# Kernel tuning notes

Hardware: AMD Instinct MI355X
Metric: run time of the kernel (lower is better)

## Reference

```python
import jax, jax.numpy as jnp
import numpy as np
import math
from jax import lax

L, E, H, F = 4, 1024, 16, 4096
B, S = 8, 512
VV, VR = 40, 30
DIST_V = 200
PAD_ID = 0


def setup_inputs() -> dict:
    key = jax.random.key(0)
    ks = iter(jax.random.split(key, 32))
    w = lambda *sh: jax.random.normal(next(ks), sh, jnp.float32) * 0.02
    inp = {
        'val_emb': w(VV, E),
        'ring_emb': w(VR, E),
        'dist_emb': w(DIST_V, H),
        'Wqkv': w(L, 3 * E, E), 'bqkv': jnp.zeros((L, 3 * E), jnp.float32),
        'Wo': w(L, E, E), 'bo': jnp.zeros((L, E), jnp.float32),
        'ln1_s': jnp.ones((L, E), jnp.float32), 'ln1_b': jnp.zeros((L, E), jnp.float32),
        'W1': w(L, F, E), 'b1': jnp.zeros((L, F), jnp.float32),
        'W2': w(L, E, F), 'b2': jnp.zeros((L, E), jnp.float32),
        'ln2_s': jnp.ones((L, E), jnp.float32), 'ln2_b': jnp.zeros((L, E), jnp.float32),
        'lnf_s': jnp.ones((E,), jnp.float32), 'lnf_b': jnp.zeros((E,), jnp.float32),
        'gen_W': w(VV * VR, E), 'gen_b': jnp.zeros((VV * VR,), jnp.float32),
    }
    val = jax.random.randint(next(ks), (B, S), 0, VV)
    val = val.at[:, 0].set(1)  # ensure first key is never <pad> (id 0)
    inp['val_sequences'] = val
    inp['ring_sequences'] = jax.random.randint(next(ks), (B, S), 0, VR)
    inp['distance_squares'] = jax.random.randint(next(ks), (B, S, S), 0, DIST_V)
    return inp


def _ln(x, s, b):
    m = x.mean(-1, keepdims=True)
    v = ((x - m) ** 2).mean(-1, keepdims=True)
    return (x - m) / jnp.sqrt(v + 1e-5) * s + b


def _forward(val_emb, ring_emb, dist_emb, Wqkv, bqkv, Wo, bo, ln1_s, ln1_b,
             W1, b1, W2, b2, ln2_s, ln2_b, lnf_s, lnf_b, gen_W, gen_b,
             val_sequences, ring_sequences, distance_squares):
    Bv, Sv = val_sequences.shape
    dh = E // H
    scale = 1.0 / math.sqrt(dh)
    # token embeddings, each scaled by sqrt(emb_size)
    x = (val_emb[val_sequences] + ring_emb[ring_sequences]) * math.sqrt(E)  # [B,S,E]
    # distance bias [B,S,S,H] -> [B,H,S,S], causal fill with -inf, key padding -inf
    bias = jnp.transpose(dist_emb[distance_squares], (0, 3, 1, 2))
    causal = jnp.tril(jnp.ones((Sv, Sv), bool))
    mask = jnp.where(causal[None, None], bias, -jnp.inf)
    pad = (val_sequences == PAD_ID)  # [B,S]
    mask = jnp.where(pad[:, None, None, :], -jnp.inf, mask)

    def step(h, p):
        wqkv, bq, wo, bo_, l1s, l1b, w1, b1_, w2, b2_, l2s, l2b = p
        qkv = h @ wqkv.T + bq  # [B,S,3E]
        q, k, v = jnp.split(qkv, 3, axis=-1)
        q = q.reshape(Bv, Sv, H, dh).transpose(0, 2, 1, 3)
        k = k.reshape(Bv, Sv, H, dh).transpose(0, 2, 1, 3)
        v = v.reshape(Bv, Sv, H, dh).transpose(0, 2, 1, 3)
        scores = jnp.einsum('bhqd,bhkd->bhqk', q, k) * scale + mask
        a = jax.nn.softmax(scores, axis=-1)
        ctx = jnp.einsum('bhqk,bhkd->bhqd', a, v)
        ctx = ctx.transpose(0, 2, 1, 3).reshape(Bv, Sv, E)
        h = _ln(h + ctx @ wo.T + bo_, l1s, l1b)  # post-norm
        ff = jax.nn.gelu(h @ w1.T + b1_, approximate=False) @ w2.T + b2_
        h = _ln(h + ff, l2s, l2b)
        return h, None

    layer_params = (Wqkv, bqkv, Wo, bo, ln1_s, ln1_b, W1, b1, W2, b2, ln2_s, ln2_b)
    x, _ = lax.scan(step, x, layer_params)
    x = _ln(x, lnf_s, lnf_b)
    return x @ gen_W.T + gen_b  # [B,S,VV*VR]


def reference(val_emb, ring_emb, dist_emb, Wqkv, bqkv, Wo, bo, ln1_s, ln1_b,
              W1, b1, W2, b2, ln2_s, ln2_b, lnf_s, lnf_b, gen_W, gen_b,
              val_sequences, ring_sequences, distance_squares):
    return _forward(val_emb, ring_emb, dist_emb, Wqkv, bqkv, Wo, bo, ln1_s, ln1_b,
                    W1, b1, W2, b2, ln2_s, ln2_b, lnf_s, lnf_b, gen_W, gen_b,
                    val_sequences, ring_sequences, distance_squares)
```

## Files before the change

kernel.cpp:

```cpp
#include <hip/hip_runtime.h>
#include <hip/hip_bf16.h>

typedef __attribute__((ext_vector_type(8))) short bf16x8;
typedef __attribute__((ext_vector_type(4))) float f32x4;
typedef unsigned short u16;
typedef __attribute__((ext_vector_type(4))) unsigned short u16x4;

#define L_ 4
#define E_ 1024
#define H_ 16
#define F_ 4096
#define B_ 8
#define S_ 512
#define T_ 4096
#define GEN_N 1200
#define GEN_PAD 1280

#define AS1 __attribute__((address_space(1)))
#define AS3 __attribute__((address_space(3)))

static __device__ __forceinline__ u16 f2bf(float f) {
  unsigned u = __float_as_uint(f);
  unsigned r = (u + 0x7fffu + ((u >> 16) & 1u)) >> 16;
  return (u16)r;
}

static __device__ __forceinline__ float fast_gelu(float v) {
  float y = 0.7978845608f * (v + 0.044715f * v * v * v);
  y = fminf(fmaxf(y, -9.f), 9.f);
  float e2 = __expf(2.f * y);
  float th = (e2 - 1.f) / (e2 + 1.f);
  return 0.5f * v * (1.f + th);
}

__global__ __launch_bounds__(256) void cvt_bf16(const float* __restrict__ src,
                                                u16* __restrict__ dst, int n) {
  int i = (blockIdx.x * 256 + threadIdx.x) * 4;
  if (i >= n) return;
  float4 v = *reinterpret_cast<const float4*>(src + i);
  u16x4 o = {f2bf(v.x), f2bf(v.y), f2bf(v.z), f2bf(v.w)};
  *reinterpret_cast<u16x4*>(dst + i) = o;
}

__global__ __launch_bounds__(256) void embed_k(const float* __restrict__ val_emb,
                                               const float* __restrict__ ring_emb,
                                               const int* __restrict__ vseq,
                                               const int* __restrict__ rseq,
                                               float* __restrict__ h, u16* __restrict__ xbf) {
  int tok = blockIdx.x;
  int e = threadIdx.x * 4;
  int v = vseq[tok], r = rseq[tok];
  float4 a = *reinterpret_cast<const float4*>(val_emb + v * E_ + e);
  float4 b = *reinterpret_cast<const float4*>(ring_emb + r * E_ + e);
  float4 o;
  o.x = (a.x + b.x) * 32.f; o.y = (a.y + b.y) * 32.f;
  o.z = (a.z + b.z) * 32.f; o.w = (a.w + b.w) * 32.f;
  *reinterpret_cast<float4*>(h + (size_t)tok * E_ + e) = o;
  u16x4 ob = {f2bf(o.x), f2bf(o.y), f2bf(o.z), f2bf(o.w)};
  *reinterpret_cast<u16x4*>(xbf + (size_t)tok * E_ + e) = ob;
}

__global__ __launch_bounds__(256) void ln_k(const float* hin, const float* add0,
                                            const float* add1, const float* cbias,
                                            const float* g, const float* bta,
                                            float* hout, u16* xout) {
  int tok = blockIdx.x;
  int e = threadIdx.x * 4;
  float4 v = *reinterpret_cast<const float4*>(hin + (size_t)tok * E_ + e);
  if (add0) {
    float4 a0 = *reinterpret_cast<const float4*>(add0 + (size_t)tok * E_ + e);
    float4 a1 = *reinterpret_cast<const float4*>(add1 + (size_t)tok * E_ + e);
    float4 cb = *reinterpret_cast<const float4*>(cbias + e);
    v.x += a0.x + a1.x + cb.x; v.y += a0.y + a1.y + cb.y;
    v.z += a0.z + a1.z + cb.z; v.w += a0.w + a1.w + cb.w;
  }
  float s = v.x + v.y + v.z + v.w;
  float q = v.x * v.x + v.y * v.y + v.z * v.z + v.w * v.w;
  #pragma unroll
  for (int off = 1; off < 64; off <<= 1) {
    s += __shfl_xor(s, off, 64);
    q += __shfl_xor(q, off, 64);
  }
  __shared__ float ls[4], lq[4];
  int wv = threadIdx.x >> 6, ln = threadIdx.x & 63;
  if (ln == 0) { ls[wv] = s; lq[wv] = q; }
  __syncthreads();
  s = ls[0] + ls[1] + ls[2] + ls[3];
  q = lq[0] + lq[1] + lq[2] + lq[3];
  float mean = s * (1.f / E_);
  float var = q * (1.f / E_) - mean * mean;
  float inv = rsqrtf(var + 1e-5f);
  float4 gg = *reinterpret_cast<const float4*>(g + e);
  float4 bb = *reinterpret_cast<const float4*>(bta + e);
  float4 o;
  o.x = (v.x - mean) * inv * gg.x + bb.x;
  o.y = (v.y - mean) * inv * gg.y + bb.y;
  o.z = (v.z - mean) * inv * gg.z + bb.z;
  o.w = (v.w - mean) * inv * gg.w + bb.w;
  if (hout) *reinterpret_cast<float4*>(hout + (size_t)tok * E_ + e) = o;
  u16x4 ob = {f2bf(o.x), f2bf(o.y), f2bf(o.z), f2bf(o.w)};
  *reinterpret_cast<u16x4*>(xout + (size_t)tok * E_ + e) = ob;
}

template <int EPI, int NW, int SPLITK>
__global__ __launch_bounds__(512, 2) void gemm_big(const u16* __restrict__ A,
                                                   const u16* __restrict__ W,
                                                   const float* __restrict__ bias,
                                                   void* __restrict__ Cp,
                                                   u16* __restrict__ Vt,
                                                   int M, int N, int K, int tilesN) {
  constexpr int BN = 64 * NW;
  __shared__ __align__(16) u16 As[2][256 * 64];
  __shared__ __align__(16) u16 Bs[2][BN * 64];
  int tid = threadIdx.x;
  int wid = tid >> 6, ln = tid & 63;
  int wm = wid >> 2, wn = wid & 3;
  int lr = ln & 15, lk = ln >> 4;
  int nwg = gridDim.x;
  int bid = blockIdx.x;
  int swz = ((nwg & 7) == 0) ? ((bid & 7) * (nwg >> 3) + (bid >> 3)) : bid;
  int sp = 0, tile = swz;
  if (SPLITK > 1) { sp = swz & (SPLITK - 1); tile = swz / SPLITK; }
  int tm = tile / tilesN, tn = tile % tilesN;
  int row0 = tm * 256, col0 = tn * BN;
  int Ks = K / SPLITK;
  int kbase = sp * Ks;

  int srow = tid >> 3;
  int schunk = ((tid & 7) ^ (srow & 7)) * 8;
  const u16* gA = A + (size_t)(row0 + srow) * K + kbase + schunk;
  const u16* gB = W + (size_t)(col0 + srow) * K + kbase + schunk;
  size_t ldsBase = (size_t)((wid << 3) * 64) * 2;

  auto stage = [&](int buf, int kt) {
    size_t ko = (size_t)kt * 64;
    #pragma unroll
    for (int i = 0; i < 4; ++i)
      __builtin_amdgcn_global_load_lds(
          (const AS1 void*)(gA + (size_t)i * 64 * K + ko),
          (AS3 void*)((char*)&As[buf][0] + ldsBase + (size_t)i * 64 * 128), 16, 0, 0);
    #pragma unroll
    for (int i = 0; i < NW; ++i)
      __builtin_amdgcn_global_load_lds(
          (const AS1 void*)(gB + (size_t)i * 64 * K + ko),
          (AS3 void*)((char*)&Bs[buf][0] + ldsBase + (size_t)i * 64 * 128), 16, 0, 0);
  };

  f32x4 acc[8][NW];
  f32x4 z = {0.f, 0.f, 0.f, 0.f};
  #pragma unroll
  for (int m = 0; m < 8; ++m)
    #pragma unroll
    for (int n = 0; n < NW; ++n) acc[m][n] = z;

  auto compute = [&](int buf) {
    #pragma unroll
    for (int s = 0; s < 2; ++s) {
      int ch = ((s * 4 + lk) ^ (lr & 7)) * 8;
      bf16x8 bfr[NW];
      #pragma unroll
      for (int n = 0; n < NW; ++n)
        bfr[n] = *reinterpret_cast<const bf16x8*>(&Bs[buf][(wn * (16 * NW) + n * 16 + lr) * 64 + ch]);
      #pragma unroll
      for (int m = 0; m < 8; ++m) {
        bf16x8 af = *reinterpret_cast<const bf16x8*>(&As[buf][(wm * 128 + m * 16 + lr) * 64 + ch]);
        #pragma unroll
        for (int n = 0; n < NW; ++n)
          acc[m][n] = __builtin_amdgcn_mfma_f32_16x16x32_bf16(af, bfr[n], acc[m][n], 0, 0, 0);
      }
    }
  };

  int nt = Ks >> 6;
  stage(0, 0);
  int cur = 0;
  for (int t = 0; t < nt; ++t) {
    if (t + 1 < nt) {
      stage(cur ^ 1, t + 1);
      if constexpr (NW == 2) asm volatile("s_waitcnt vmcnt(6)" ::: "memory");
      else if constexpr (NW == 3) asm volatile("s_waitcnt vmcnt(7)" ::: "memory");
      else asm volatile("s_waitcnt vmcnt(8)" ::: "memory");
    } else {
      asm volatile("s_waitcnt vmcnt(0)" ::: "memory");
    }
    __builtin_amdgcn_s_barrier();
    asm volatile("" ::: "memory");
    compute(cur);
    asm volatile("" ::: "memory");
    __builtin_amdgcn_s_barrier();
    cur ^= 1;
  }

  #pragma unroll
  for (int n = 0; n < NW; ++n) {
    int col = col0 + wn * (16 * NW) + n * 16 + lr;
    if (col >= N) continue;
    float bv = (EPI == 2) ? 0.f : bias[col];
    #pragma unroll
    for (int m = 0; m < 8; ++m) {
      int rbase = row0 + wm * 128 + m * 16 + lk * 4;
      #pragma unroll
      for (int r2 = 0; r2 < 4; ++r2) {
        float v = acc[m][n][r2] + bv;
        if (EPI == 1) v = fast_gelu(v);
        int row = rbase + r2;
        if (EPI == 2)
          ((float*)Cp)[(size_t)sp * M * N + (size_t)row * N + col] = v;
        else if (EPI == 3)
          ((float*)Cp)[(size_t)row * N + col] = v;
        else {
          u16 bw = f2bf(v);
          ((u16*)Cp)[(size_t)row * N + col] = bw;
          if (EPI == 0 && Vt != nullptr && col >= 2 * E_) {
            int dg = col - 2 * E_;
            int hh = dg >> 6, dd = dg & 63;
            int bb = row >> 9, ss = row & 511;
            Vt[((size_t)((bb * 16 + hh) * 64 + dd) << 9) + ss] = bw;
          }
        }
      }
    }
  }
}

__global__ __launch_bounds__(256, 4) void attn_scores_k(const u16* __restrict__ qkv,
                                                        const int* __restrict__ dist,
                                                        const float* __restrict__ dist_emb,
                                                        const int* __restrict__ vseq,
                                                        u16* __restrict__ P,
                                                        float* __restrict__ invl) {
  int blk = blockIdx.x;
  int bh = blk & 127;
  int qt = blk >> 7;
  int b = bh >> 4, h = bh & 15;
  int tid = threadIdx.x, wv = tid >> 6, ln = tid & 63;
  int lr = ln & 15, lk = ln >> 4;

  __shared__ float de[208];
  __shared__ unsigned char padf[512];
  __shared__ unsigned char d8[64 * 512];

  int ncol = (qt + 1) * 64;
  for (int i = tid; i < 208; i += 256)
    de[i] = (i < 200) ? dist_emb[i * H_ + h] : -1e30f;
  for (int i = tid; i < (ncol >> 2); i += 256) {
    int4 v = *reinterpret_cast<const int4*>(vseq + b * S_ + i * 4);
    uchar4 pz;
    pz.x = (v.x == 0); pz.y = (v.y == 0); pz.z = (v.z == 0); pz.w = (v.w == 0);
    *reinterpret_cast<uchar4*>(&padf[i * 4]) = pz;
  }
  __syncthreads();

  {
    int r = tid >> 2;
    const int* drow = dist + ((size_t)(b * S_ + qt * 64 + r) << 9);
    int nc4 = ncol >> 2;
    for (int c4 = (tid & 3); c4 < nc4; c4 += 4) {
      int4 dv = *reinterpret_cast<const int4*>(drow + c4 * 4);
      uchar4 o;
      o.x = padf[c4 * 4 + 0] ? (unsigned char)200 : (unsigned char)dv.x;
      o.y = padf[c4 * 4 + 1] ? (unsigned char)200 : (unsigned char)dv.y;
      o.z = padf[c4 * 4 + 2] ? (unsigned char)200 : (unsigned char)dv.z;
      o.w = padf[c4 * 4 + 3] ? (unsigned char)200 : (unsigned char)dv.w;
      *reinterpret_cast<uchar4*>(&d8[(r << 9) + c4 * 4]) = o;
    }
  }
  __syncthreads();

  int q0 = qt * 64 + wv * 16;
  int nv = 4 * qt + wv + 1;
  int nreq = 4 * qt + 2 * (wv >> 1) + 2;
  int qrow = q0 + lk * 4;
  int lrow = wv * 16 + lk * 4;

  bf16x8 aq0 = *reinterpret_cast<const bf16x8*>(
      qkv + (size_t)(b * S_ + q0 + lr) * 3072 + h * 64 + lk * 8);
  bf16x8 aq1 = *reinterpret_cast<const bf16x8*>(
      qkv + (size_t)(b * S_ + q0 + lr) * 3072 + h * 64 + 32 + lk * 8);

  float sm[4] = {0.f, 0.f, 0.f, 0.f};
  f32x4 z = {0.f, 0.f, 0.f, 0.f};
  int nch = (nv + 3) >> 2;
  #pragma unroll 1
  for (int c = 0; c < nch; ++c) {
    int base = c * 4;
    f32x4 acc[4] = {z, z, z, z};
    #pragma unroll
    for (int j = 0; j < 4; ++j) {
      int n = base + j;
      if (n < nv) {
        const u16* kb = qkv + (size_t)(b * S_ + n * 16 + lr) * 3072 + E_ + h * 64 + lk * 8;
        bf16x8 bk0 = *reinterpret_cast<const bf16x8*>(kb);
        bf16x8 bk1 = *reinterpret_cast<const bf16x8*>(kb + 32);
        acc[j] = __builtin_amdgcn_mfma_f32_16x16x32_bf16(aq0, bk0, acc[j], 0, 0, 0);
        acc[j] = __builtin_amdgcn_mfma_f32_16x16x32_bf16(aq1, bk1, acc[j], 0, 0, 0);
      }
    }
    #pragma unroll
    for (int j = 0; j < 4; ++j) {
      int n = base + j;
      if (n < nv) {
        int col = n * 16 + lr;
        #pragma unroll
        for (int r2 = 0; r2 < 4; ++r2) {
          float e = 0.f;
          if (col <= qrow + r2) {
            int d = d8[((lrow + r2) << 9) + col];
            e = __expf(acc[j][r2] * 0.125f + de[d]);
          }
          sm[r2] += e;
          P[(size_t)(bh * S_ + qrow + r2) * S_ + col] = f2bf(e);
        }
      }
    }
  }
  for (int n = nv; n < nreq; ++n) {
    int col = n * 16 + lr;
    #pragma unroll
    for (int r2 = 0; r2 < 4; ++r2)
      P[(size_t)(bh * S_ + qrow + r2) * S_ + col] = 0;
  }
  #pragma unroll
  for (int off = 1; off < 16; off <<= 1)
    #pragma unroll
    for (int r2 = 0; r2 < 4; ++r2) sm[r2] += __shfl_xor(sm[r2], off, 64);
  if (lr == 0) {
    #pragma unroll
    for (int r2 = 0; r2 < 4; ++r2)
      invl[bh * S_ + qrow + r2] = 1.f / sm[r2];
  }
}

__global__ __launch_bounds__(256) void attn_pv_k(const u16* __restrict__ P,
                                                 const u16* __restrict__ Vt,
                                                 const float* __restrict__ invl,
                                                 u16* __restrict__ ctx) {
  int blk = blockIdx.x;
  int mt = blk & 3, bh = blk >> 2;
  int b = bh >> 4, h = bh & 15;
  int tid = threadIdx.x, wv = tid >> 6, ln = tid & 63;
  int lr = ln & 15, lk = ln >> 4;
  int r0 = mt * 128 + wv * 32;
  f32x4 acc[2][4];
  f32x4 z = {0.f, 0.f, 0.f, 0.f};
  #pragma unroll
  for (int m = 0; m < 2; ++m)
    #pragma unroll
    for (int n = 0; n < 4; ++n) acc[m][n] = z;
  int nks = mt * 4 + wv + 1;
  for (int ks = 0; ks < nks; ++ks) {
    int k0 = ks * 32;
    bf16x8 ap[2];
    #pragma unroll
    for (int m = 0; m < 2; ++m)
      ap[m] = *reinterpret_cast<const bf16x8*>(
          P + (size_t)(bh * S_ + r0 + m * 16 + lr) * S_ + k0 + lk * 8);
    #pragma unroll
    for (int n = 0; n < 4; ++n) {
      bf16x8 bv = *reinterpret_cast<const bf16x8*>(
          Vt + (size_t)(bh * 64 + n * 16 + lr) * S_ + k0 + lk * 8);
      #pragma unroll
      for (int m = 0; m < 2; ++m)
        acc[m][n] = __builtin_amdgcn_mfma_f32_16x16x32_bf16(ap[m], bv, acc[m][n], 0, 0, 0);
    }
  }
  float il[2][4];
  #pragma unroll
  for (int m = 0; m < 2; ++m)
    #pragma unroll
    for (int r = 0; r < 4; ++r)
      il[m][r] = invl[bh * S_ + r0 + m * 16 + lk * 4 + r];
  #pragma unroll
  for (int m = 0; m < 2; ++m)
    #pragma unroll
    for (int n = 0; n < 4; ++n)
      #pragma unroll
      for (int r = 0; r < 4; ++r) {
        int row = r0 + m * 16 + lk * 4 + r;
        int col = n * 16 + lr;
        ctx[(size_t)(b * S_ + row) * E_ + h * 64 + col] = f2bf(acc[m][n][r] * il[m][r]);
      }
}

extern "C" void kernel_launch(void* const* d_in, const int* in_sizes, int n_in,
                              void* d_out, int out_size, void* d_ws, size_t ws_size,
                              hipStream_t stream) {
  const float* val_emb = (const float*)d_in[0];
  const float* ring_emb = (const float*)d_in[1];
  const float* dist_emb = (const float*)d_in[2];
  const float* Wqkv = (const float*)d_in[3];
  const float* bqkv = (const float*)d_in[4];
  const float* Wo = (const float*)d_in[5];
  const float* bo = (const float*)d_in[6];
  const float* ln1_s = (const float*)d_in[7];
  const float* ln1_b = (const float*)d_in[8];
  const float* W1 = (const float*)d_in[9];
  const float* b1 = (const float*)d_in[10];
  const float* W2 = (const float*)d_in[11];
  const float* b2 = (const float*)d_in[12];
  const float* ln2_s = (const float*)d_in[13];
  const float* ln2_b = (const float*)d_in[14];
  const float* lnf_s = (const float*)d_in[15];
  const float* lnf_b = (const float*)d_in[16];
  const float* gen_W = (const float*)d_in[17];
  const float* gen_b = (const float*)d_in[18];
  const int* vseq = (const int*)d_in[19];
  const int* rseq = (const int*)d_in[20];
  const int* dist = (const int*)d_in[21];

  char* ws = (char*)d_ws;
  size_t off = 0;
  auto alloc = [&](size_t nbytes) {
    char* p = ws + off;
    off += (nbytes + 255) & ~(size_t)255;
    return p;
  };
  u16* gw_bf = (u16*)alloc((size_t)GEN_PAD * E_ * 2);
  u16* wqkv_l = (u16*)alloc((size_t)3 * E_ * E_ * 2);
  u16* wo_l = (u16*)alloc((size_t)E_ * E_ * 2);
  u16* w1_l = (u16*)alloc((size_t)F_ * E_ * 2);
  u16* w2_l = (u16*)alloc((size_t)E_ * F_ * 2);
  float* h = (float*)alloc((size_t)T_ * E_ * 4);
  u16* x_bf = (u16*)alloc((size_t)T_ * E_ * 2);
  u16* qkv_bf = (u16*)alloc((size_t)T_ * 3 * E_ * 2);
  u16* ctx_bf = (u16*)alloc((size_t)T_ * E_ * 2);
  u16* vt_bf = (u16*)alloc((size_t)B_ * H_ * 64 * S_ * 2);
  float* invl = (float*)alloc((size_t)B_ * H_ * S_ * 4);
  u16* p_bf = (u16*)alloc((size_t)B_ * H_ * S_ * S_ * 2);
  u16* ff_bf = p_bf;
  float* psum = (float*)(p_bf + (size_t)T_ * F_);
  (void)ws_size; (void)in_sizes; (void)n_in; (void)out_size; (void)rseq;

  auto cvt = [&](const float* s, u16* d, int n) {
    cvt_bf16<<<dim3((n / 4 + 255) / 256), dim3(256), 0, stream>>>(s, d, n);
  };
  cvt(gen_W, gw_bf, GEN_N * E_);

  embed_k<<<dim3(T_), dim3(256), 0, stream>>>(val_emb, ring_emb, vseq, rseq, h, x_bf);

  for (int l = 0; l < L_; ++l) {
    cvt(Wqkv + (size_t)l * 3 * E_ * E_, wqkv_l, 3 * E_ * E_);
    cvt(Wo + (size_t)l * E_ * E_, wo_l, E_ * E_);
    cvt(W1 + (size_t)l * F_ * E_, w1_l, F_ * E_);
    cvt(W2 + (size_t)l * E_ * F_, w2_l, E_ * F_);

    gemm_big<0, 3, 1><<<dim3(256), dim3(512), 0, stream>>>(
        x_bf, wqkv_l, bqkv + (size_t)l * 3 * E_, qkv_bf, vt_bf, T_, 3 * E_, E_, 16);
    attn_scores_k<<<dim3(B_ * H_ * 8), dim3(256), 0, stream>>>(qkv_bf, dist, dist_emb, vseq,
                                                               p_bf, invl);
    attn_pv_k<<<dim3(B_ * H_ * 4), dim3(256), 0, stream>>>(p_bf, vt_bf, invl, ctx_bf);
    gemm_big<2, 2, 2><<<dim3(256), dim3(512), 0, stream>>>(
        ctx_bf, wo_l, nullptr, psum, nullptr, T_, E_, E_, 8);
    ln_k<<<dim3(T_), dim3(256), 0, stream>>>(h, psum, psum + (size_t)T_ * E_,
                                             bo + (size_t)l * E_,
                                             ln1_s + (size_t)l * E_, ln1_b + (size_t)l * E_,
                                             h, x_bf);
    gemm_big<1, 4, 1><<<dim3(256), dim3(512), 0, stream>>>(
        x_bf, w1_l, b1 + (size_t)l * F_, ff_bf, nullptr, T_, F_, E_, 16);
    gemm_big<2, 2, 2><<<dim3(256), dim3(512), 0, stream>>>(
        ff_bf, w2_l, nullptr, psum, nullptr, T_, E_, F_, 8);
    ln_k<<<dim3(T_), dim3(256), 0, stream>>>(h, psum, psum + (size_t)T_ * E_,
                                             b2 + (size_t)l * E_,
                                             ln2_s + (size_t)l * E_, ln2_b + (size_t)l * E_,
                                             h, x_bf);
  }
  ln_k<<<dim3(T_), dim3(256), 0, stream>>>(h, nullptr, nullptr, nullptr, lnf_s, lnf_b,
                                           nullptr, x_bf);
  gemm_big<3, 2, 1><<<dim3(160), dim3(512), 0, stream>>>(
      x_bf, gw_bf, gen_b, (float*)d_out, nullptr, T_, GEN_N, E_, 10);
}
```

Measured before the change: 1.161 ms.

## Add 256x256-tile GEMM with split-K-stage pipelining for QKV and FFN layers

Adds a new gemm8 kernel that uses 256x256 output tiles, an XOR-swizzled LDS layout, and direct global-to-LDS loads. Each 64-wide K step is split into two 32-wide halves so the next half's load overlaps the current compute, and MFMA issue priority is raised during compute. The QKV, FFN1 and FFN2 GEMMs switch to it. FFN2 now uses 4-way split-K, with two extra partial buffers placed in the qkv buffer and summed in a widened LayerNorm kernel. Tradeoffs are fewer workgroups for QKV (192), higher register pressure from the larger accumulator, and extra partial-sum memory traffic for FFN2.

New measurement: 1.180 ms. Within noise of the previous version (+1.6%).

```diff
diff --git a/kernel.cpp b/kernel.cpp
--- a/kernel.cpp
+++ b/kernel.cpp
@@ -61,7 +61,8 @@
 }
 
 __global__ __launch_bounds__(256) void ln_k(const float* hin, const float* add0,
-                                            const float* add1, const float* cbias,
+                                            const float* add1, const float* add2,
+                                            const float* add3, const float* cbias,
                                             const float* g, const float* bta,
                                             float* hout, u16* xout) {
   int tok = blockIdx.x;
@@ -73,6 +74,12 @@
     float4 cb = *reinterpret_cast<const float4*>(cbias + e);
     v.x += a0.x + a1.x + cb.x; v.y += a0.y + a1.y + cb.y;
     v.z += a0.z + a1.z + cb.z; v.w += a0.w + a1.w + cb.w;
+    if (add2) {
+      float4 a2 = *reinterpret_cast<const float4*>(add2 + (size_t)tok * E_ + e);
+      float4 a3 = *reinterpret_cast<const float4*>(add3 + (size_t)tok * E_ + e);
+      v.x += a2.x + a3.x; v.y += a2.y + a3.y;
+      v.z += a2.z + a3.z; v.w += a2.w + a3.w;
+    }
   }
   float s = v.x + v.y + v.z + v.w;
   float q = v.x * v.x + v.y * v.y + v.z * v.z + v.w * v.w;
@@ -100,6 +107,145 @@
   if (hout) *reinterpret_cast<float4*>(hout + (size_t)tok * E_ + e) = o;
   u16x4 ob = {f2bf(o.x), f2bf(o.y), f2bf(o.z), f2bf(o.w)};
   *reinterpret_cast<u16x4*>(xout + (size_t)tok * E_ + e) = ob;
+}
+
+template <int EPI, int SPLITK>
+__global__ __launch_bounds__(512, 2) void gemm8(const u16* __restrict__ A,
+                                                const u16* __restrict__ W,
+                                                const float* __restrict__ bias,
+                                                void* __restrict__ Cp,
+                                                float* __restrict__ Cp2,
+                                                u16* __restrict__ Vt,
+                                                int M, int N, int K, int tilesN) {
+  __shared__ __align__(16) char lds[131072];
+  int tid = threadIdx.x;
+  int wid = tid >> 6, l = tid & 63;
+  int wm = wid >> 2, wn = wid & 3, bh = wn >> 1;
+  int lr = l & 15, lk = l >> 4;
+  int su = wid & 3;
+  int sb = (wid & 1) | ((wid >> 2) << 1);
+  int nwg = gridDim.x, bid = blockIdx.x;
+  int swz = ((nwg & 7) == 0) ? ((bid & 7) * (nwg >> 3) + (bid >> 3)) : bid;
+  int sp = 0, tile = swz;
+  if (SPLITK > 1) { sp = swz & (SPLITK - 1); tile = swz / SPLITK; }
+  int tm = tile / tilesN, tn = tile % tilesN;
+  int row0 = tm * 256, col0 = tn * 256;
+  int Ks = K / SPLITK, kbase = sp * Ks;
+
+  int arow0 = row0 + wm * 128 + su * 32 + (l >> 2);
+  int brow0 = col0 + bh * 128 + sb * 32 + (l >> 2);
+  int sch = ((l & 3) ^ ((l >> 2) & 3)) * 8;
+  const u16* gA0 = A + (size_t)arow0 * K + kbase + sch;
+  const u16* gA1 = A + (size_t)(arow0 + 16) * K + kbase + sch;
+  const u16* gB0 = W + (size_t)brow0 * K + kbase + sch;
+  const u16* gB1 = W + (size_t)(brow0 + 16) * K + kbase + sch;
+  int dA = wm * 16384 + su * 2048;
+  int dB = 65536 + bh * 16384 + sb * 2048;
+
+  auto stageU = [&](int buf, int s, int kt) {
+    size_t ko = (size_t)kt * 64 + s * 32;
+    int bo = buf * 32768 + s * 8192;
+    __builtin_amdgcn_global_load_lds((const AS1 void*)(gA0 + ko),
+                                     (AS3 void*)(lds + dA + bo), 16, 0, 0);
+    __builtin_amdgcn_global_load_lds((const AS1 void*)(gA1 + ko),
+                                     (AS3 void*)(lds + dA + bo + 1024), 16, 0, 0);
+    __builtin_amdgcn_global_load_lds((const AS1 void*)(gB0 + ko),
+                                     (AS3 void*)(lds + dB + bo), 16, 0, 0);
+    __builtin_amdgcn_global_load_lds((const AS1 void*)(gB1 + ko),
+                                     (AS3 void*)(lds + dB + bo + 1024), 16, 0, 0);
+  };
+
+  int rsw = (lk ^ (lr & 3)) * 16;
+  f32x4 acc[8][4];
+  f32x4 z = {0.f, 0.f, 0.f, 0.f};
+  #pragma unroll
+  for (int m = 0; m < 8; ++m)
+    #pragma unroll
+    for (int n = 0; n < 4; ++n) acc[m][n] = z;
+
+  int nt = Ks >> 6;
+  stageU(0, 0, 0);
+  stageU(0, 1, 0);
+  for (int t = 0; t < nt; ++t) {
+    int buf = t & 1;
+    int aoff = buf * 32768 + wm * 16384;
+    int boff = 65536 + buf * 32768 + bh * 16384 + (wn & 1) * 4096;
+    if (t + 1 < nt) {
+      stageU(buf ^ 1, 0, t + 1);
+      asm volatile("s_waitcnt vmcnt(4)" ::: "memory");
+    } else {
+      asm volatile("s_waitcnt vmcnt(0)" ::: "memory");
+    }
+    __builtin_amdgcn_s_barrier();
+    asm volatile("" ::: "memory");
+    {
+      bf16x8 bfr[4], af[8];
+      #pragma unroll
+      for (int n = 0; n < 4; ++n)
+        bfr[n] = *reinterpret_cast<const bf16x8*>(lds + boff + (n * 16 + lr) * 64 + rsw);
+      #pragma unroll
+      for (int m = 0; m < 8; ++m)
+        af[m] = *reinterpret_cast<const bf16x8*>(lds + aoff + (m * 16 + lr) * 64 + rsw);
+      __builtin_amdgcn_s_setprio(1);
+      #pragma unroll
+      for (int m = 0; m < 8; ++m)
+        #pragma unroll
+        for (int n = 0; n < 4; ++n)
+          acc[m][n] = __builtin_amdgcn_mfma_f32_16x16x32_bf16(af[m], bfr[n], acc[m][n], 0, 0, 0);
+      __builtin_amdgcn_s_setprio(0);
+    }
+    if (t + 1 < nt) stageU(buf ^ 1, 1, t + 1);
+    asm volatile("" ::: "memory");
+    __builtin_amdgcn_s_barrier();
+    asm volatile("" ::: "memory");
+    {
+      bf16x8 bfr[4], af[8];
+      #pragma unroll
+      for (int n = 0; n < 4; ++n)
+        bfr[n] = *reinterpret_cast<const bf16x8*>(lds + boff + 8192 + (n * 16 + lr) * 64 + rsw);
+      #pragma unroll
+      for (int m = 0; m < 8; ++m)
+        af[m] = *reinterpret_cast<const bf16x8*>(lds + aoff + 8192 + (m * 16 + lr) * 64 + rsw);
+      __builtin_amdgcn_s_setprio(1);
+      #pragma unroll
+      for (int m = 0; m < 8; ++m)
+        #pragma unroll
+        for (int n = 0; n < 4; ++n)
+          acc[m][n] = __builtin_amdgcn_mfma_f32_16x16x32_bf16(af[m], bfr[n], acc[m][n], 0, 0, 0);
+      __builtin_amdgcn_s_setprio(0);
+    }
+    asm volatile("" ::: "memory");
+  }
+
+  #pragma unroll
+  for (int n = 0; n < 4; ++n) {
+    int col = col0 + wn * 64 + n * 16 + lr;
+    if (col >= N) continue;
+    float bv = (EPI == 2) ? 0.f : bias[col];
+    #pragma unroll
+    for (int m = 0; m < 8; ++m) {
+      int rbase = row0 + wm * 128 + m * 16 + lk * 4;
+      #pragma unroll
+      for (int r2 = 0; r2 < 4; ++r2) {
+        float v = acc[m][n][r2] + bv;
+        if (EPI == 1) v = fast_gelu(v);
+        int row = rbase + r2;
+        if (EPI == 2) {
+          float* dst = (sp < 2) ? (float*)Cp : Cp2;
+          dst[(size_t)(sp & 1) * M * N + (size_t)row * N + col] = v;
+        } else {
+          u16 bw = f2bf(v);
+          ((u16*)Cp)[(size_t)row * N + col] = bw;
+          if (EPI == 0 && Vt != nullptr && col >= 2 * E_) {
+            int dg = col - 2 * E_;
+            int hh = dg >> 6, dd = dg & 63;
+            int bb = row >> 9, ss = row & 511;
+            Vt[((size_t)((bb * 16 + hh) * 64 + dd) << 9) + ss] = bw;
+          }
+        }
+      }
+    }
+  }
 }
 
 template <int EPI, int NW, int SPLITK>
@@ -178,7 +324,6 @@
     if (t + 1 < nt) {
       stage(cur ^ 1, t + 1);
       if constexpr (NW == 2) asm volatile("s_waitcnt vmcnt(6)" ::: "memory");
-      else if constexpr (NW == 3) asm volatile("s_waitcnt vmcnt(7)" ::: "memory");
       else asm volatile("s_waitcnt vmcnt(8)" ::: "memory");
     } else {
       asm volatile("s_waitcnt vmcnt(0)" ::: "memory");
@@ -202,25 +347,15 @@
       #pragma unroll
       for (int r2 = 0; r2 < 4; ++r2) {
         float v = acc[m][n][r2] + bv;
-        if (EPI == 1) v = fast_gelu(v);
         int row = rbase + r2;
         if (EPI == 2)
           ((float*)Cp)[(size_t)sp * M * N + (size_t)row * N + col] = v;
-        else if (EPI == 3)
+        else
           ((float*)Cp)[(size_t)row * N + col] = v;
-        else {
-          u16 bw = f2bf(v);
-          ((u16*)Cp)[(size_t)row * N + col] = bw;
-          if (EPI == 0 && Vt != nullptr && col >= 2 * E_) {
-            int dg = col - 2 * E_;
-            int hh = dg >> 6, dd = dg & 63;
-            int bb = row >> 9, ss = row & 511;
-            Vt[((size_t)((bb * 16 + hh) * 64 + dd) << 9) + ss] = bw;
-          }
-        }
       }
     }
   }
+  (void)Vt;
 }
 
 __global__ __launch_bounds__(256, 4) void attn_scores_k(const u16* __restrict__ qkv,
@@ -429,6 +564,7 @@
   u16* p_bf = (u16*)alloc((size_t)B_ * H_ * S_ * S_ * 2);
   u16* ff_bf = p_bf;
   float* psum = (float*)(p_bf + (size_t)T_ * F_);
+  float* psum2 = (float*)qkv_bf;
   (void)ws_size; (void)in_sizes; (void)n_in; (void)out_size; (void)rseq;
 
   auto cvt = [&](const float* s, u16* d, int n) {
@@ -444,28 +580,29 @@
     cvt(W1 + (size_t)l * F_ * E_, w1_l, F_ * E_);
     cvt(W2 + (size_t)l * E_ * F_, w2_l, E_ * F_);
 
-    gemm_big<0, 3, 1><<<dim3(256), dim3(512), 0, stream>>>(
-        x_bf, wqkv_l, bqkv + (size_t)l * 3 * E_, qkv_bf, vt_bf, T_, 3 * E_, E_, 16);
+    gemm8<0, 1><<<dim3(192), dim3(512), 0, stream>>>(
+        x_bf, wqkv_l, bqkv + (size_t)l * 3 * E_, qkv_bf, nullptr, vt_bf, T_, 3 * E_, E_, 12);
     attn_scores_k<<<dim3(B_ * H_ * 8), dim3(256), 0, stream>>>(qkv_bf, dist, dist_emb, vseq,
                                                                p_bf, invl);
     attn_pv_k<<<dim3(B_ * H_ * 4), dim3(256), 0, stream>>>(p_bf, vt_bf, invl, ctx_bf);
     gemm_big<2, 2, 2><<<dim3(256), dim3(512), 0, stream>>>(
         ctx_bf, wo_l, nullptr, psum, nullptr, T_, E_, E_, 8);
     ln_k<<<dim3(T_), dim3(256), 0, stream>>>(h, psum, psum + (size_t)T_ * E_,
-                                             bo + (size_t)l * E_,
+                                             nullptr, nullptr, bo + (size_t)l * E_,
                                              ln1_s + (size_t)l * E_, ln1_b + (size_t)l * E_,
                                              h, x_bf);
-    gemm_big<1, 4, 1><<<dim3(256), dim3(512), 0, stream>>>(
-        x_bf, w1_l, b1 + (size_t)l * F_, ff_bf, nullptr, T_, F_, E_, 16);
-    gemm_big<2, 2, 2><<<dim3(256), dim3(512), 0, stream>>>(
-        ff_bf, w2_l, nullptr, psum, nullptr, T_, E_, F_, 8);
+    gemm8<1, 1><<<dim3(256), dim3(512), 0, stream>>>(
+        x_bf, w1_l, b1 + (size_t)l * F_, ff_bf, nullptr, nullptr, T_, F_, E_, 16);
+    gemm8<2, 4><<<dim3(256), dim3(512), 0, stream>>>(
+        ff_bf, w2_l, nullptr, psum, psum2, nullptr, T_, E_, F_, 4);
     ln_k<<<dim3(T_), dim3(256), 0, stream>>>(h, psum, psum + (size_t)T_ * E_,
+                                             psum2, psum2 + (size_t)T_ * E_,
                                              b2 + (size_t)l * E_,
                                              ln2_s + (size_t)l * E_, ln2_b + (size_t)l * E_,
                                              h, x_bf);
   }
-  ln_k<<<dim3(T_), dim3(256), 0, stream>>>(h, nullptr, nullptr, nullptr, lnf_s, lnf_b,
-                                           nullptr, x_bf);
+  ln_k<<<dim3(T_), dim3(256), 0, stream>>>(h, nullptr, nullptr, nullptr, nullptr, nullptr,
+                                           lnf_s, lnf_b, nullptr, x_bf);
   gemm_big<3, 2, 1><<<dim3(160), dim3(512), 0, stream>>>(
       x_bf, gw_bf, gen_b, (float*)d_out, nullptr, T_, GEN_N, E_, 10);
 }
```

## Fuse attention scores and PV into one kernel keeping probabilities in registers

Applied to the files above, without the earlier changes.

Merges the score/softmax kernel and the PV kernel into a single fused attention kernel. It computes S transposed so each lane holds key-major probabilities, then packs them to bf16 and shuffles them across lanes into an MFMA A-fragment, accumulating P·V directly without writing P to global memory. This removes the large bf16 P round trip through HBM and one kernel launch per layer, and pads the LDS distance tile to avoid bank conflicts. The cost is extra cross-lane shuffles and less PV parallelism, since each block now does its query tile's full causal range serially.

Measured after the change: 1.086 ms. 6.4% less time.

```diff
diff --git a/kernel.cpp b/kernel.cpp
--- a/kernel.cpp
+++ b/kernel.cpp
@@ -23,6 +23,12 @@
   unsigned u = __float_as_uint(f);
   unsigned r = (u + 0x7fffu + ((u >> 16) & 1u)) >> 16;
   return (u16)r;
+}
+
+static __device__ __forceinline__ unsigned cvt_pk_bf16(float lo, float hi) {
+  unsigned r;
+  asm("v_cvt_pk_bf16_f32 %0, %1, %2" : "=v"(r) : "v"(lo), "v"(hi));
+  return r;
 }
 
 static __device__ __forceinline__ float fast_gelu(float v) {
@@ -223,22 +229,22 @@
   }
 }
 
-__global__ __launch_bounds__(256, 4) void attn_scores_k(const u16* __restrict__ qkv,
-                                                        const int* __restrict__ dist,
-                                                        const float* __restrict__ dist_emb,
-                                                        const int* __restrict__ vseq,
-                                                        u16* __restrict__ P,
-                                                        float* __restrict__ invl) {
+__global__ __launch_bounds__(256, 4) void attn_fused_k(const u16* __restrict__ qkv,
+                                                       const int* __restrict__ dist,
+                                                       const float* __restrict__ dist_emb,
+                                                       const int* __restrict__ vseq,
+                                                       const u16* __restrict__ Vt,
+                                                       u16* __restrict__ ctx) {
   int blk = blockIdx.x;
   int bh = blk & 127;
   int qt = blk >> 7;
   int b = bh >> 4, h = bh & 15;
-  int tid = threadIdx.x, wv = tid >> 6, ln = tid & 63;
-  int lr = ln & 15, lk = ln >> 4;
+  int tid = threadIdx.x, wv = tid >> 6, l = tid & 63;
+  int lr = l & 15, lk = l >> 4;
 
   __shared__ float de[208];
   __shared__ unsigned char padf[512];
-  __shared__ unsigned char d8[64 * 512];
+  __shared__ unsigned char d8[64 * 516];
 
   int ncol = (qt + 1) * 64;
   for (int i = tid; i < 208; i += 256)
@@ -262,124 +268,108 @@
       o.y = padf[c4 * 4 + 1] ? (unsigned char)200 : (unsigned char)dv.y;
       o.z = padf[c4 * 4 + 2] ? (unsigned char)200 : (unsigned char)dv.z;
       o.w = padf[c4 * 4 + 3] ? (unsigned char)200 : (unsigned char)dv.w;
-      *reinterpret_cast<uchar4*>(&d8[(r << 9) + c4 * 4]) = o;
+      *reinterpret_cast<uchar4*>(&d8[r * 516 + c4 * 4]) = o;
     }
   }
   __syncthreads();
 
   int q0 = qt * 64 + wv * 16;
   int nv = 4 * qt + wv + 1;
-  int nreq = 4 * qt + 2 * (wv >> 1) + 2;
-  int qrow = q0 + lk * 4;
-  int lrow = wv * 16 + lk * 4;
+  int qglob = q0 + lr;
+  int qloc = wv * 16 + lr;
 
   bf16x8 aq0 = *reinterpret_cast<const bf16x8*>(
       qkv + (size_t)(b * S_ + q0 + lr) * 3072 + h * 64 + lk * 8);
   bf16x8 aq1 = *reinterpret_cast<const bf16x8*>(
       qkv + (size_t)(b * S_ + q0 + lr) * 3072 + h * 64 + 32 + lk * 8);
 
-  float sm[4] = {0.f, 0.f, 0.f, 0.f};
+  float sm = 0.f;
   f32x4 z = {0.f, 0.f, 0.f, 0.f};
-  int nch = (nv + 3) >> 2;
+  f32x4 acc_o[4] = {z, z, z, z};
+
+  int sA = lr + ((2 * lk) & 3) * 16;
+  int sB = lr + ((2 * lk + 1) & 3) * 16;
+  int jsel = (lk >= 2);
+
+  int ngroups = (nv + 1) >> 1;
   #pragma unroll 1
-  for (int c = 0; c < nch; ++c) {
-    int base = c * 4;
-    f32x4 acc[4] = {z, z, z, z};
-    #pragma unroll
-    for (int j = 0; j < 4; ++j) {
-      int n = base + j;
-      if (n < nv) {
-        const u16* kb = qkv + (size_t)(b * S_ + n * 16 + lr) * 3072 + E_ + h * 64 + lk * 8;
-        bf16x8 bk0 = *reinterpret_cast<const bf16x8*>(kb);
-        bf16x8 bk1 = *reinterpret_cast<const bf16x8*>(kb + 32);
-        acc[j] = __builtin_amdgcn_mfma_f32_16x16x32_bf16(aq0, bk0, acc[j], 0, 0, 0);
-        acc[j] = __builtin_amdgcn_mfma_f32_16x16x32_bf16(aq1, bk1, acc[j], 0, 0, 0);
+  for (int g = 0; g < ngroups; ++g) {
+    f32x4 s0 = z, s1 = z;
+    {
+      int n = 2 * g;
+      const u16* kb = qkv + (size_t)(b * S_ + n * 16 + lr) * 3072 + E_ + h * 64 + lk * 8;
+      bf16x8 bk0 = *reinterpret_cast<const bf16x8*>(kb);
+      bf16x8 bk1 = *reinterpret_cast<const bf16x8*>(kb + 32);
+      s0 = __builtin_amdgcn_mfma_f32_16x16x32_bf16(bk0, aq0, s0, 0, 0, 0);
+      s0 = __builtin_amdgcn_mfma_f32_16x16x32_bf16(bk1, aq1, s0, 0, 0, 0);
+    }
+    if (2 * g + 1 < nv) {
+      int n = 2 * g + 1;
+      const u16* kb = qkv + (size_t)(b * S_ + n * 16 + lr) * 3072 + E_ + h * 64 + lk * 8;
+      bf16x8 bk0 = *reinterpret_cast<const bf16x8*>(kb);
+      bf16x8 bk1 = *reinterpret_cast<const bf16x8*>(kb + 32);
+      s1 = __builtin_amdgcn_mfma_f32_16x16x32_bf16(bk0, aq0, s1, 0, 0, 0);
+      s1 = __builtin_amdgcn_mfma_f32_16x16x32_bf16(bk1, aq1, s1, 0, 0, 0);
+    }
+    float e0[4], e1[4];
+    #pragma unroll
+    for (int r2 = 0; r2 < 4; ++r2) {
+      int kg0 = (2 * g) * 16 + lk * 4 + r2;
+      float e = 0.f;
+      if (kg0 <= qglob) {
+        int d = d8[qloc * 516 + kg0];
+        e = __expf(s0[r2] * 0.125f + de[d]);
       }
-    }
-    #pragma unroll
-    for (int j = 0; j < 4; ++j) {
-      int n = base + j;
-      if (n < nv) {
-        int col = n * 16 + lr;
-        #pragma unroll
-        for (int r2 = 0; r2 < 4; ++r2) {
-          float e = 0.f;
-          if (col <= qrow + r2) {
-            int d = d8[((lrow + r2) << 9) + col];
-            e = __expf(acc[j][r2] * 0.125f + de[d]);
-          }
-          sm[r2] += e;
-          P[(size_t)(bh * S_ + qrow + r2) * S_ + col] = f2bf(e);
-        }
+      e0[r2] = e; sm += e;
+    }
+    #pragma unroll
+    for (int r2 = 0; r2 < 4; ++r2) {
+      int kg1 = (2 * g + 1) * 16 + lk * 4 + r2;
+      float e = 0.f;
+      if (2 * g + 1 < nv && kg1 <= qglob) {
+        int d = d8[qloc * 516 + kg1];
+        e = __expf(s1[r2] * 0.125f + de[d]);
       }
-    }
-  }
-  for (int n = nv; n < nreq; ++n) {
-    int col = n * 16 + lr;
-    #pragma unroll
-    for (int r2 = 0; r2 < 4; ++r2)
-      P[(size_t)(bh * S_ + qrow + r2) * S_ + col] = 0;
-  }
+      e1[r2] = e; sm += e;
+    }
+    unsigned t0p0 = cvt_pk_bf16(e0[0], e0[1]);
+    unsigned t0p1 = cvt_pk_bf16(e0[2], e0[3]);
+    unsigned t1p0 = cvt_pk_bf16(e1[0], e1[1]);
+    unsigned t1p1 = cvt_pk_bf16(e1[2], e1[3]);
+    unsigned a00 = __shfl((int)t0p0, sA, 64), a10 = __shfl((int)t1p0, sA, 64);
+    unsigned a01 = __shfl((int)t0p1, sA, 64), a11 = __shfl((int)t1p1, sA, 64);
+    unsigned b00 = __shfl((int)t0p0, sB, 64), b10 = __shfl((int)t1p0, sB, 64);
+    unsigned b01 = __shfl((int)t0p1, sB, 64), b11 = __shfl((int)t1p1, sB, 64);
+    unsigned w0 = jsel ? a10 : a00;
+    unsigned w1 = jsel ? a11 : a01;
+    unsigned w2 = jsel ? b10 : b00;
+    unsigned w3 = jsel ? b11 : b01;
+    bf16x8 pfrag;
+    {
+      unsigned pw[4] = {w0, w1, w2, w3};
+      pfrag = *reinterpret_cast<bf16x8*>(pw);
+    }
+    #pragma unroll
+    for (int n4 = 0; n4 < 4; ++n4) {
+      bf16x8 vf = *reinterpret_cast<const bf16x8*>(
+          Vt + (size_t)(bh * 64 + n4 * 16 + lr) * S_ + g * 32 + lk * 8);
+      acc_o[n4] = __builtin_amdgcn_mfma_f32_16x16x32_bf16(vf, pfrag, acc_o[n4], 0, 0, 0);
+    }
+  }
+
+  sm += __shfl_xor(sm, 16, 64);
+  sm += __shfl_xor(sm, 32, 64);
+  float il = 1.f / sm;
+
   #pragma unroll
-  for (int off = 1; off < 16; off <<= 1)
-    #pragma unroll
-    for (int r2 = 0; r2 < 4; ++r2) sm[r2] += __shfl_xor(sm[r2], off, 64);
-  if (lr == 0) {
-    #pragma unroll
-    for (int r2 = 0; r2 < 4; ++r2)
-      invl[bh * S_ + qrow + r2] = 1.f / sm[r2];
-  }
-}
-
-__global__ __launch_bounds__(256) void attn_pv_k(const u16* __restrict__ P,
-                                                 const u16* __restrict__ Vt,
-                                                 const float* __restrict__ invl,
-                                                 u16* __restrict__ ctx) {
-  int blk = blockIdx.x;
-  int mt = blk & 3, bh = blk >> 2;
-  int b = bh >> 4, h = bh & 15;
-  int tid = threadIdx.x, wv = tid >> 6, ln = tid & 63;
-  int lr = ln & 15, lk = ln >> 4;
-  int r0 = mt * 128 + wv * 32;
-  f32x4 acc[2][4];
-  f32x4 z = {0.f, 0.f, 0.f, 0.f};
-  #pragma unroll
-  for (int m = 0; m < 2; ++m)
-    #pragma unroll
-    for (int n = 0; n < 4; ++n) acc[m][n] = z;
-  int nks = mt * 4 + wv + 1;
-  for (int ks = 0; ks < nks; ++ks) {
-    int k0 = ks * 32;
-    bf16x8 ap[2];
-    #pragma unroll
-    for (int m = 0; m < 2; ++m)
-      ap[m] = *reinterpret_cast<const bf16x8*>(
-          P + (size_t)(bh * S_ + r0 + m * 16 + lr) * S_ + k0 + lk * 8);
-    #pragma unroll
-    for (int n = 0; n < 4; ++n) {
-      bf16x8 bv = *reinterpret_cast<const bf16x8*>(
-          Vt + (size_t)(bh * 64 + n * 16 + lr) * S_ + k0 + lk * 8);
-      #pragma unroll
-      for (int m = 0; m < 2; ++m)
-        acc[m][n] = __builtin_amdgcn_mfma_f32_16x16x32_bf16(ap[m], bv, acc[m][n], 0, 0, 0);
-    }
-  }
-  float il[2][4];
-  #pragma unroll
-  for (int m = 0; m < 2; ++m)
-    #pragma unroll
-    for (int r = 0; r < 4; ++r)
-      il[m][r] = invl[bh * S_ + r0 + m * 16 + lk * 4 + r];
-  #pragma unroll
-  for (int m = 0; m < 2; ++m)
-    #pragma unroll
-    for (int n = 0; n < 4; ++n)
-      #pragma unroll
-      for (int r = 0; r < 4; ++r) {
-        int row = r0 + m * 16 + lk * 4 + r;
-        int col = n * 16 + lr;
-        ctx[(size_t)(b * S_ + row) * E_ + h * 64 + col] = f2bf(acc[m][n][r] * il[m][r]);
-      }
+  for (int n4 = 0; n4 < 4; ++n4) {
+    u16x4 o;
+    o.x = f2bf(acc_o[n4][0] * il);
+    o.y = f2bf(acc_o[n4][1] * il);
+    o.z = f2bf(acc_o[n4][2] * il);
+    o.w = f2bf(acc_o[n4][3] * il);
+    *reinterpret_cast<u16x4*>(ctx + (size_t)(b * S_ + qglob) * E_ + h * 64 + n4 * 16 + lk * 4) = o;
+  }
 }
 
 extern "C" void kernel_launch(void* const* d_in, const int* in_sizes, int n_in,
@@ -425,7 +415,6 @@
   u16* qkv_bf = (u16*)alloc((size_t)T_ * 3 * E_ * 2);
   u16* ctx_bf = (u16*)alloc((size_t)T_ * E_ * 2);
   u16* vt_bf = (u16*)alloc((size_t)B_ * H_ * 64 * S_ * 2);
-  float* invl = (float*)alloc((size_t)B_ * H_ * S_ * 4);
   u16* p_bf = (u16*)alloc((size_t)B_ * H_ * S_ * S_ * 2);
   u16* ff_bf = p_bf;
   float* psum = (float*)(p_bf + (size_t)T_ * F_);
@@ -446,9 +435,8 @@
 
     gemm_big<0, 3, 1><<<dim3(256), dim3(512), 0, stream>>>(
         x_bf, wqkv_l, bqkv + (size_t)l * 3 * E_, qkv_bf, vt_bf, T_, 3 * E_, E_, 16);
-    attn_scores_k<<<dim3(B_ * H_ * 8), dim3(256), 0, stream>>>(qkv_bf, dist, dist_emb, vseq,
-                                                               p_bf, invl);
-    attn_pv_k<<<dim3(B_ * H_ * 4), dim3(256), 0, stream>>>(p_bf, vt_bf, invl, ctx_bf);
+    attn_fused_k<<<dim3(B_ * H_ * 8), dim3(256), 0, stream>>>(qkv_bf, dist, dist_emb,
+                                                              vseq, vt_bf, ctx_bf);
     gemm_big<2, 2, 2><<<dim3(256), dim3(512), 0, stream>>>(
         ctx_bf, wo_l, nullptr, psum, nullptr, T_, E_, E_, 8);
     ln_k<<<dim3(T_), dim3(256), 0, stream>>>(h, psum, psum + (size_t)T_ * E_,
```
